# Kernel tuning notes

Measured on AMD Instinct MI355X. Metric: run time of the kernel, lower is better.

## Reference

```python
import jax, jax.numpy as jnp
import numpy as np

N, D, H = 500000, 128, 128
B, M = 1024, 512


def setup_inputs() -> dict:
    key = jax.random.key(0)
    k = jax.random.split(key, 8)
    return {
        "embed": jax.random.normal(k[0], (N, D), dtype=jnp.float32),
        "node_feat": jax.random.normal(k[1], (N, D), dtype=jnp.float32),
        "W1": jax.random.normal(k[2], (2 * D, H), dtype=jnp.float32) * 0.05,
        "b1": jnp.zeros((H,), dtype=jnp.float32),
        "W2": jax.random.normal(k[3], (H, 1), dtype=jnp.float32) * 0.05,
        "b2": jnp.zeros((1,), dtype=jnp.float32),
        "query_idx": jax.random.randint(k[4], (B,), 0, N),
        "cand_idx": jax.random.randint(k[5], (B, M), 0, N),
        "top_k": 3,
    }


def reference(embed, node_feat, W1, b1, W2, b2, query_idx, cand_idx, top_k):
    # Gather query and candidate (k-hop subgraph) embeddings.
    q = embed[query_idx]                                   # [B, D]
    c = embed[cand_idx]                                    # [B, M, D]
    Bv, Mv, Dv = c.shape
    pair = jnp.concatenate(
        [jnp.broadcast_to(q[:, None, :], (Bv, Mv, Dv)), c], axis=-1
    )                                                      # [B, M, 2D]
    # Tiny 2-layer MLP edge scorer (one fused pass over all edges).
    h = jax.nn.relu(jnp.einsum("bmf,fh->bmh", pair, W1) + b1)
    scores = (jnp.einsum("bmh,ho->bmo", h, W2) + b2)[..., 0]  # [B, M]
    # Sort-based top-k selection (original sorted per-etype lists).
    _, pos = jax.lax.top_k(scores, top_k)                  # [B, k]
    top_nodes = jnp.take_along_axis(cand_idx, pos, axis=1) # [B, k]
    # Zero out features of the selected nodes (hard mask), as in original.
    masked_feat = node_feat.at[top_nodes.reshape(-1)].set(0.0)
    return scores, masked_feat
```

## Files before the change

kernel.cpp:

```cpp
#include <hip/hip_runtime.h>
#include <math.h>

#define D 128
#define H 128
#define BQ 1024
#define M 512
#define NNODES 500000
#define K_MAX 8
#define SHORT 16
#define NSCORE BQ
#define NCOPY 2048
#define COPY_N4 ((long)NNODES * D / 4)
#define CSTRIDE ((long)NCOPY * 256)

typedef __attribute__((ext_vector_type(8))) short bf16x8;
typedef __attribute__((ext_vector_type(4))) float f32x4;
typedef __attribute__((ext_vector_type(4))) unsigned u32x4;

static __device__ __forceinline__ unsigned pack2bf(float a, float b) {
    unsigned ua = __float_as_uint(a);
    unsigned ub = __float_as_uint(b);
    ua = ua + 0x7fffu + ((ua >> 16) & 1u);
    ub = ub + 0x7fffu + ((ub >> 16) & 1u);
    return (ua >> 16) | (ub & 0xffff0000u);
}

__global__ void wconv_kernel(const float* __restrict__ W1,
                             unsigned short* __restrict__ wTswz) {
    const int idx = blockIdx.x * 256 + threadIdx.x;
    const int h = idx >> 7;
    const int inner = (idx & 127) * 2;
    const int k = (inner ^ ((h & 7) << 4)) >> 1;
    const float v = W1[(long)(D + k) * H + h];
    wTswz[idx] = (unsigned short)pack2bf(v, 0.f);
}

__global__ void qproj_kernel(const float* __restrict__ embed,
                             const float* __restrict__ W1,
                             const float* __restrict__ b1,
                             const int* __restrict__ query_idx,
                             float* __restrict__ qh) {
    __shared__ float qrow[D];
    const int b = blockIdx.x;
    const int t = threadIdx.x;
    const long qi = query_idx[b];
    qrow[t] = embed[qi * D + t];
    __syncthreads();
    float acc = b1[t];
#pragma unroll 8
    for (int d = 0; d < D; ++d)
        acc = fmaf(qrow[d], W1[d * H + t], acc);
    qh[b * H + t] = acc;
}

__global__ __launch_bounds__(256, 4)
void fused_kernel(const float* __restrict__ embed,
                  const unsigned short* __restrict__ wTswz,
                  const float* __restrict__ W2,
                  const float* __restrict__ b2,
                  const int* __restrict__ cand_idx,
                  const float* __restrict__ qh,
                  float* __restrict__ scores,
                  const f32x4* __restrict__ nf_src,
                  f32x4* __restrict__ nf_dst) {
    __shared__ __align__(16) char Bs[32768];
    const int bid = blockIdx.x;
    const int t   = threadIdx.x;
    const int r3  = bid % 3;

    if (r3 != 1) {
        const int cid = (bid / 3) * 2 + (r3 >> 1);
        long i = (long)cid * 256 + t;
        for (; i + 3 * CSTRIDE < COPY_N4; i += 4 * CSTRIDE) {
            const f32x4 v0 = __builtin_nontemporal_load(&nf_src[i]);
            const f32x4 v1 = __builtin_nontemporal_load(&nf_src[i + CSTRIDE]);
            const f32x4 v2 = __builtin_nontemporal_load(&nf_src[i + 2 * CSTRIDE]);
            const f32x4 v3 = __builtin_nontemporal_load(&nf_src[i + 3 * CSTRIDE]);
            __builtin_nontemporal_store(v0, &nf_dst[i]);
            __builtin_nontemporal_store(v1, &nf_dst[i + CSTRIDE]);
            __builtin_nontemporal_store(v2, &nf_dst[i + 2 * CSTRIDE]);
            __builtin_nontemporal_store(v3, &nf_dst[i + 3 * CSTRIDE]);
        }
        for (; i < COPY_N4; i += CSTRIDE) {
            const f32x4 v = __builtin_nontemporal_load(&nf_src[i]);
            __builtin_nontemporal_store(v, &nf_dst[i]);
        }
        return;
    }

    const int b = bid / 3;

    {
#pragma unroll
        for (int i = 0; i < 8; ++i) {
            const int c = i * 256 + t;
            const uint4 v = ((const uint4*)wTswz)[c];
            *(uint4*)(Bs + (size_t)c * 16) = v;
        }
    }

    const int lane = t & 63;
    const int w    = t >> 6;
    const int g    = lane >> 4;
    const int c    = lane & 15;
    const int sw   = (c & 7) << 4;

    float qv[8], w2[8];
#pragma unroll
    for (int cb = 0; cb < 8; ++cb) {
        qv[cb] = qh[b * H + cb * 16 + c];
        w2[cb] = W2[cb * 16 + c];
    }
    const float b2v = b2[0];

    int idx[8];
    const int ibase = b * M + w * 16 + c;
#pragma unroll
    for (int mt = 0; mt < 8; ++mt) idx[mt] = cand_idx[ibase + mt * 64];

    __syncthreads();

    f32x4 buf[8];
    {
        const float* rp = embed + (long)idx[0] * D + g * 8;
#pragma unroll
        for (int ks = 0; ks < 4; ++ks) {
            buf[2 * ks]     = *(const f32x4*)(rp + ks * 32);
            buf[2 * ks + 1] = *(const f32x4*)(rp + ks * 32 + 4);
        }
    }

#pragma unroll
    for (int mt = 0; mt < 8; ++mt) {
        bf16x8 afr[4];
#pragma unroll
        for (int ks = 0; ks < 4; ++ks) {
            u32x4 u;
            u.x = pack2bf(buf[2 * ks].x, buf[2 * ks].y);
            u.y = pack2bf(buf[2 * ks].z, buf[2 * ks].w);
            u.z = pack2bf(buf[2 * ks + 1].x, buf[2 * ks + 1].y);
            u.w = pack2bf(buf[2 * ks + 1].z, buf[2 * ks + 1].w);
            afr[ks] = __builtin_bit_cast(bf16x8, u);
        }
        if (mt < 7) {
            const float* rp = embed + (long)idx[mt + 1] * D + g * 8;
#pragma unroll
            for (int ks = 0; ks < 4; ++ks) {
                buf[2 * ks]     = *(const f32x4*)(rp + ks * 32);
                buf[2 * ks + 1] = *(const f32x4*)(rp + ks * 32 + 4);
            }
        }

        f32x4 acc[8];
#pragma unroll
        for (int cb = 0; cb < 8; ++cb) acc[cb] = (f32x4){0.f, 0.f, 0.f, 0.f};
#pragma unroll
        for (int ks = 0; ks < 4; ++ks) {
            const int koff = (ks * 64 + g * 16) ^ sw;
#pragma unroll
            for (int cb = 0; cb < 8; ++cb) {
                const bf16x8 bv = *(const bf16x8*)(Bs + ((cb * 16 + c) << 8) + koff);
                acc[cb] = __builtin_amdgcn_mfma_f32_16x16x32_bf16(afr[ks], bv, acc[cb], 0, 0, 0);
            }
        }

        float s0 = 0.f, s1 = 0.f, s2 = 0.f, s3 = 0.f;
#pragma unroll
        for (int cb = 0; cb < 8; ++cb) {
            s0 = fmaf(fmaxf(qv[cb] + acc[cb][0], 0.f), w2[cb], s0);
            s1 = fmaf(fmaxf(qv[cb] + acc[cb][1], 0.f), w2[cb], s1);
            s2 = fmaf(fmaxf(qv[cb] + acc[cb][2], 0.f), w2[cb], s2);
            s3 = fmaf(fmaxf(qv[cb] + acc[cb][3], 0.f), w2[cb], s3);
        }
#pragma unroll
        for (int off = 1; off <= 8; off <<= 1) {
            s0 += __shfl_xor(s0, off);
            s1 += __shfl_xor(s1, off);
            s2 += __shfl_xor(s2, off);
            s3 += __shfl_xor(s3, off);
        }
        if (c == 0) {
            float* out = scores + b * M + mt * 64 + w * 16 + g * 4;
            out[0] = s0 + b2v;
            out[1] = s1 + b2v;
            out[2] = s2 + b2v;
            out[3] = s3 + b2v;
        }
    }
}

__global__ void topk16_kernel(const float* __restrict__ scores,
                              int* __restrict__ shortpos) {
    const int b = blockIdx.x;
    const int lane = threadIdx.x;
    const float* row = scores + b * M;
    float v[8];
    {
        const float4 x0 = ((const float4*)row)[lane * 2];
        const float4 x1 = ((const float4*)row)[lane * 2 + 1];
        v[0] = x0.x; v[1] = x0.y; v[2] = x0.z; v[3] = x0.w;
        v[4] = x1.x; v[5] = x1.y; v[6] = x1.z; v[7] = x1.w;
    }
    for (int kk = 0; kk < SHORT; ++kk) {
        float bv = v[0];
        int bi = lane * 8;
#pragma unroll
        for (int j = 1; j < 8; ++j)
            if (v[j] > bv) { bv = v[j]; bi = lane * 8 + j; }
#pragma unroll
        for (int off = 32; off >= 1; off >>= 1) {
            const float ov = __shfl_xor(bv, off);
            const int   oi = __shfl_xor(bi, off);
            if (ov > bv || (ov == bv && oi < bi)) { bv = ov; bi = oi; }
        }
        if (lane == 0) shortpos[b * SHORT + kk] = bi;
        if ((bi >> 3) == lane) v[bi & 7] = -3.402823466e38f;
    }
}

__global__ __launch_bounds__(128)
void refine_kernel(const float* __restrict__ embed,
                   const float* __restrict__ W1,
                   const float* __restrict__ W2,
                   const float* __restrict__ qh,
                   const int* __restrict__ cand_idx,
                   const int* __restrict__ shortpos,
                   const int* __restrict__ topk_ptr,
                   int* __restrict__ top_nodes) {
    __shared__ float crows[SHORT][D];
    __shared__ float red[SHORT][D];
    __shared__ int spos[SHORT];
    const int b = blockIdx.x;
    const int t = threadIdx.x;

    if (t < SHORT) spos[t] = shortpos[b * SHORT + t];
    __syncthreads();
    {
        const int cc = t >> 3;
        const int d0 = (t & 7) * 16;
        const long node = cand_idx[b * M + spos[cc]];
        const float4* rp = (const float4*)(embed + node * D);
        float4* wp = (float4*)&crows[cc][d0];
#pragma unroll
        for (int j = 0; j < 4; ++j) wp[j] = rp[d0 / 4 + j];
    }
    __syncthreads();

    float acc[SHORT];
#pragma unroll
    for (int cc = 0; cc < SHORT; ++cc) acc[cc] = 0.f;
    const float* W1bot = W1 + (long)D * H;
    for (int d = 0; d < D; ++d) {
        const float w1v = W1bot[d * H + t];
#pragma unroll
        for (int cc = 0; cc < SHORT; ++cc)
            acc[cc] = fmaf(crows[cc][d], w1v, acc[cc]);
    }
    const float qv = qh[b * H + t];
    const float w2 = W2[t];
#pragma unroll
    for (int cc = 0; cc < SHORT; ++cc)
        red[cc][t] = fmaxf(qv + acc[cc], 0.f) * w2;
    __syncthreads();

    if (t < 64) {
#pragma unroll
        for (int cc = 0; cc < SHORT; ++cc) {
            float v = red[cc][t] + red[cc][t + 64];
#pragma unroll
            for (int off = 32; off >= 1; off >>= 1) v += __shfl_xor(v, off);
            if (t == 0) red[cc][0] = v;
        }
    }
    __syncthreads();

    if (t == 0) {
        int k = *topk_ptr;
        if (k > K_MAX) k = K_MAX;
        unsigned used = 0;
        for (int kk = 0; kk < K_MAX; ++kk) {
            if (kk < k) {
                int best = -1, bpos = 0x7fffffff;
                float bv = 0.f;
                for (int cc = 0; cc < SHORT; ++cc) {
                    if (used & (1u << cc)) continue;
                    const float v = red[cc][0];
                    const int p = spos[cc];
                    if (best < 0 || v > bv || (v == bv && p < bpos)) {
                        best = cc; bv = v; bpos = p;
                    }
                }
                used |= 1u << best;
                top_nodes[b * K_MAX + kk] = cand_idx[b * M + bpos];
            } else {
                top_nodes[b * K_MAX + kk] = -1;
            }
        }
    }
}

__global__ void zero_rows_kernel(const int* __restrict__ top_nodes,
                                 float* __restrict__ masked) {
    const int node = top_nodes[blockIdx.x];
    if (node < 0) return;
    masked[(long)node * D + threadIdx.x] = 0.f;
}

extern "C" void kernel_launch(void* const* d_in, const int* in_sizes, int n_in,
                              void* d_out, int out_size, void* d_ws, size_t ws_size,
                              hipStream_t stream) {
    const float* embed     = (const float*)d_in[0];
    const float* node_feat = (const float*)d_in[1];
    const float* W1        = (const float*)d_in[2];
    const float* b1        = (const float*)d_in[3];
    const float* W2        = (const float*)d_in[4];
    const float* b2        = (const float*)d_in[5];
    const int*   query_idx = (const int*)d_in[6];
    const int*   cand_idx  = (const int*)d_in[7];
    const int*   topk_ptr  = (const int*)d_in[8];

    float* scores = (float*)d_out;
    float* masked = (float*)d_out + (long)BQ * M;

    char* p = (char*)d_ws;
    float*          qh        = (float*)p;          p += (long)BQ * H * 4;
    int*            shortpos  = (int*)p;            p += (long)BQ * SHORT * 4;
    int*            top_nodes = (int*)p;            p += (long)BQ * K_MAX * 4;
    unsigned short* wTswz     = (unsigned short*)p;

    wconv_kernel<<<(H * D) / 256, 256, 0, stream>>>(W1, wTswz);
    qproj_kernel<<<BQ, H, 0, stream>>>(embed, W1, b1, query_idx, qh);

    fused_kernel<<<NSCORE + NCOPY, 256, 0, stream>>>(
        embed, wTswz, W2, b2, cand_idx, qh, scores,
        (const f32x4*)node_feat, (f32x4*)masked);

    topk16_kernel<<<BQ, 64, 0, stream>>>(scores, shortpos);
    refine_kernel<<<BQ, 128, 0, stream>>>(embed, W1, W2, qh, cand_idx,
                                          shortpos, topk_ptr, top_nodes);
    zero_rows_kernel<<<BQ * K_MAX, D, 0, stream>>>(top_nodes, masked);
}
```

Baseline: 182.6 us.

## Split scoring blocks in half, double-buffer gathers, widen LDS swizzle

Each batch row's scoring now runs on two blocks covering 256 candidates each, so there are twice as many scoring blocks. Embedding gathers are double-buffered two rows ahead, which puts more loads in flight per wave. The LDS XOR swizzle widens from 8 to 16 rows to reduce bank conflicts on B-fragment reads. Copy and score blocks now alternate one-to-one instead of 2:1, and each scoring block reloads the 32KB weight tile, doubling that traffic.

Measured after the change: 197.7 us. 8.3% more time.

```diff
diff --git a/kernel.cpp b/kernel.cpp
--- a/kernel.cpp
+++ b/kernel.cpp
@@ -8,7 +8,7 @@
 #define NNODES 500000
 #define K_MAX 8
 #define SHORT 16
-#define NSCORE BQ
+#define NSCORE (BQ * 2)
 #define NCOPY 2048
 #define COPY_N4 ((long)NNODES * D / 4)
 #define CSTRIDE ((long)NCOPY * 256)
@@ -30,7 +30,7 @@
     const int idx = blockIdx.x * 256 + threadIdx.x;
     const int h = idx >> 7;
     const int inner = (idx & 127) * 2;
-    const int k = (inner ^ ((h & 7) << 4)) >> 1;
+    const int k = (inner ^ ((h & 15) << 4)) >> 1;
     const float v = W1[(long)(D + k) * H + h];
     wTswz[idx] = (unsigned short)pack2bf(v, 0.f);
 }
@@ -52,6 +52,19 @@
         acc = fmaf(qrow[d], W1[d * H + t], acc);
     qh[b * H + t] = acc;
 }
+
+#define GATHER(BUF, NODE)                                                    \
+    {                                                                        \
+        const float* rp_ = embed + (long)(NODE) * D + g * 8;                 \
+        BUF[0] = *(const f32x4*)(rp_);                                       \
+        BUF[1] = *(const f32x4*)(rp_ + 4);                                   \
+        BUF[2] = *(const f32x4*)(rp_ + 32);                                  \
+        BUF[3] = *(const f32x4*)(rp_ + 36);                                  \
+        BUF[4] = *(const f32x4*)(rp_ + 64);                                  \
+        BUF[5] = *(const f32x4*)(rp_ + 68);                                  \
+        BUF[6] = *(const f32x4*)(rp_ + 96);                                  \
+        BUF[7] = *(const f32x4*)(rp_ + 100);                                 \
+    }
 
 __global__ __launch_bounds__(256, 4)
 void fused_kernel(const float* __restrict__ embed,
@@ -66,10 +79,9 @@
     __shared__ __align__(16) char Bs[32768];
     const int bid = blockIdx.x;
     const int t   = threadIdx.x;
-    const int r3  = bid % 3;
-
-    if (r3 != 1) {
-        const int cid = (bid / 3) * 2 + (r3 >> 1);
+
+    if ((bid & 1) == 0) {
+        const int cid = bid >> 1;
         long i = (long)cid * 256 + t;
         for (; i + 3 * CSTRIDE < COPY_N4; i += 4 * CSTRIDE) {
             const f32x4 v0 = __builtin_nontemporal_load(&nf_src[i]);
@@ -88,7 +100,9 @@
         return;
     }
 
-    const int b = bid / 3;
+    const int sid  = bid >> 1;
+    const int b    = sid >> 1;
+    const int half = sid & 1;
 
     {
 #pragma unroll
@@ -103,7 +117,7 @@
     const int w    = t >> 6;
     const int g    = lane >> 4;
     const int c    = lane & 15;
-    const int sw   = (c & 7) << 4;
+    const int sw   = c << 4;
 
     float qv[8], w2[8];
 #pragma unroll
@@ -113,43 +127,33 @@
     }
     const float b2v = b2[0];
 
-    int idx[8];
-    const int ibase = b * M + w * 16 + c;
-#pragma unroll
-    for (int mt = 0; mt < 8; ++mt) idx[mt] = cand_idx[ibase + mt * 64];
-
-    __syncthreads();
-
-    f32x4 buf[8];
-    {
-        const float* rp = embed + (long)idx[0] * D + g * 8;
+    int idx[4];
+    const int ibase = b * M + half * 256 + w * 16 + c;
+#pragma unroll
+    for (int mt = 0; mt < 4; ++mt) idx[mt] = cand_idx[ibase + mt * 64];
+
+    __syncthreads();
+
+    f32x4 bufA[8], bufB[8];
+    GATHER(bufA, idx[0]);
+    GATHER(bufB, idx[1]);
+
+#pragma unroll
+    for (int mt = 0; mt < 4; ++mt) {
+        bf16x8 afr[4];
 #pragma unroll
         for (int ks = 0; ks < 4; ++ks) {
-            buf[2 * ks]     = *(const f32x4*)(rp + ks * 32);
-            buf[2 * ks + 1] = *(const f32x4*)(rp + ks * 32 + 4);
-        }
-    }
-
-#pragma unroll
-    for (int mt = 0; mt < 8; ++mt) {
-        bf16x8 afr[4];
-#pragma unroll
-        for (int ks = 0; ks < 4; ++ks) {
+            const f32x4 lo = (mt & 1) ? bufB[2 * ks]     : bufA[2 * ks];
+            const f32x4 hi = (mt & 1) ? bufB[2 * ks + 1] : bufA[2 * ks + 1];
             u32x4 u;
-            u.x = pack2bf(buf[2 * ks].x, buf[2 * ks].y);
-            u.y = pack2bf(buf[2 * ks].z, buf[2 * ks].w);
-            u.z = pack2bf(buf[2 * ks + 1].x, buf[2 * ks + 1].y);
-            u.w = pack2bf(buf[2 * ks + 1].z, buf[2 * ks + 1].w);
+            u.x = pack2bf(lo.x, lo.y);
+            u.y = pack2bf(lo.z, lo.w);
+            u.z = pack2bf(hi.x, hi.y);
+            u.w = pack2bf(hi.z, hi.w);
             afr[ks] = __builtin_bit_cast(bf16x8, u);
         }
-        if (mt < 7) {
-            const float* rp = embed + (long)idx[mt + 1] * D + g * 8;
-#pragma unroll
-            for (int ks = 0; ks < 4; ++ks) {
-                buf[2 * ks]     = *(const f32x4*)(rp + ks * 32);
-                buf[2 * ks + 1] = *(const f32x4*)(rp + ks * 32 + 4);
-            }
-        }
+        if (mt == 0) GATHER(bufA, idx[2]);
+        if (mt == 1) GATHER(bufB, idx[3]);
 
         f32x4 acc[8];
 #pragma unroll
@@ -180,7 +184,7 @@
             s3 += __shfl_xor(s3, off);
         }
         if (c == 0) {
-            float* out = scores + b * M + mt * 64 + w * 16 + g * 4;
+            float* out = scores + b * M + half * 256 + mt * 64 + w * 16 + g * 4;
             out[0] = s0 + b2v;
             out[1] = s1 + b2v;
             out[2] = s2 + b2v;
```
